# Performance work log

Measured on AMD Instinct MI355X. Metric: run time of the kernel, lower is better.

The kernel has to match this reference:

```python
import jax, jax.numpy as jnp
import numpy as np

N = 50000       # nodes
E = 1600000     # edges (avg degree 32)
DIN = 64
DOUT = 64
DE = 16
ATT_SLOPE = 0.2   # leaky_relu slope inside attention (GAT standard)
ACT_SLOPE = 0.01  # F.leaky_relu default between layers


def setup_inputs() -> dict:
    key = jax.random.key(0)
    ks = jax.random.split(key, 16)

    def lin(k, i, o):
        return jax.random.normal(k, (i, o), jnp.float32) / np.sqrt(i).astype(np.float32)

    def vec(k, d):
        return jax.random.normal(k, (d,), jnp.float32) / np.sqrt(d).astype(np.float32)

    return {
        "X": jax.random.normal(ks[0], (N, DIN), jnp.float32),
        "edge_index": jax.random.randint(ks[1], (2, E), 0, N),
        "edge_attr": jax.random.normal(ks[2], (E, DE), jnp.float32),
        # layer 1 params
        "W1": lin(ks[3], DIN, DOUT), "We1": lin(ks[4], DE, DOUT),
        "as1": vec(ks[5], DOUT), "ad1": vec(ks[6], DOUT), "ae1": vec(ks[7], DOUT),
        "b1": jnp.zeros((DOUT,), jnp.float32),
        # layer 2 params
        "W2": lin(ks[8], DOUT, DOUT), "We2": lin(ks[9], DE, DOUT),
        "as2": vec(ks[10], DOUT), "ad2": vec(ks[11], DOUT), "ae2": vec(ks[12], DOUT),
        "b2": jnp.zeros((DOUT,), jnp.float32),
    }


def _gat_conv(x, src, dst, edge_attr, W, We, a_s, a_d, a_e, b):
    """GATConv with edge features, softmax attention over dst neighborhoods, max aggregation."""
    n = x.shape[0]
    h = x @ W                      # [N, DOUT]
    e = edge_attr @ We             # [E, DOUT]
    # per-edge attention logits
    logits = jax.nn.leaky_relu((h @ a_s)[src] + (h @ a_d)[dst] + e @ a_e, ATT_SLOPE)  # [E]
    # numerically-stable segment softmax over destination node
    m = jax.ops.segment_max(logits, dst, num_segments=n)      # [N]
    p = jnp.exp(logits - m[dst])                               # [E]
    s = jax.ops.segment_sum(p, dst, num_segments=n)            # [N]
    att = p / jnp.maximum(s[dst], 1e-16)                       # [E]
    msg = (h[src] + e) * att[:, None]                          # [E, DOUT]
    out = jax.ops.segment_max(msg, dst, num_segments=n)        # [N, DOUT], -inf for empty
    out = jnp.where(jnp.isfinite(out), out, 0.0)
    return out + b


def reference(X, edge_index, edge_attr,
              W1, We1, as1, ad1, ae1, b1,
              W2, We2, as2, ad2, ae2, b2):
    src, dst = edge_index[0], edge_index[1]
    c1 = _gat_conv(X, src, dst, edge_attr, W1, We1, as1, ad1, ae1, b1)
    c1 = jax.nn.leaky_relu(c1, ACT_SLOPE)
    c2 = _gat_conv(c1, src, dst, edge_attr, W2, We2, as2, ad2, ae2, b2)
    c2 = jax.nn.leaky_relu(c2, ACT_SLOPE)
    return c2
```

## Files before the change

kernel.cpp:

```cpp
#include <hip/hip_runtime.h>
#include <cstdint>
#include <cstddef>

#define NN 50000
#define EE 1600000
#define D  64
#define DE 16

typedef __attribute__((ext_vector_type(2))) float vf2;

__device__ __forceinline__ float bf2f(unsigned short u) {
    return __uint_as_float(((unsigned)u) << 16);
}
__device__ __forceinline__ unsigned short f2bf(float f) {
    unsigned u = __float_as_uint(f);
    unsigned r = u + 0x7FFFu + ((u >> 16) & 1u);
    return (unsigned short)(r >> 16);
}
__device__ __forceinline__ vf2 vmax2(vf2 a, vf2 b) {
    vf2 r; r.x = fmaxf(a.x, b.x); r.y = fmaxf(a.y, b.y); return r;
}

__global__ __launch_bounds__(256) void k_hist(const int* dst, int* counts) {
    int e = blockIdx.x * 256 + threadIdx.x;
    if (e < EE) atomicAdd(&counts[dst[e]], 1);
}

__global__ __launch_bounds__(256) void k_scanA(const int* counts, int* bsum) {
    __shared__ int tmp[256];
    int t = threadIdx.x, i = blockIdx.x * 256 + t;
    tmp[t] = (i < NN) ? counts[i] : 0;
    __syncthreads();
    for (int off = 128; off; off >>= 1) {
        if (t < off) tmp[t] += tmp[t + off];
        __syncthreads();
    }
    if (t == 0) bsum[blockIdx.x] = tmp[0];
}

__global__ __launch_bounds__(256) void k_scanB(int* bsum, int nchunks) {
    __shared__ int tmp[256];
    int t = threadIdx.x;
    int v = (t < nchunks) ? bsum[t] : 0;
    tmp[t] = v; __syncthreads();
    for (int off = 1; off < 256; off <<= 1) {
        int x = (t >= off) ? tmp[t - off] : 0;
        __syncthreads();
        tmp[t] += x;
        __syncthreads();
    }
    if (t < nchunks) bsum[t] = tmp[t] - v;
}

__global__ __launch_bounds__(256) void k_scanC(const int* counts, const int* bsumex,
                                               int* offsets, int* cursor) {
    __shared__ int tmp[256];
    int t = threadIdx.x, i = blockIdx.x * 256 + t;
    int v = (i < NN) ? counts[i] : 0;
    tmp[t] = v; __syncthreads();
    for (int off = 1; off < 256; off <<= 1) {
        int x = (t >= off) ? tmp[t - off] : 0;
        __syncthreads();
        tmp[t] += x;
        __syncthreads();
    }
    int excl = tmp[t] - v + bsumex[blockIdx.x];
    if (i < NN) { offsets[i] = excl; cursor[i] = excl; }
}

__global__ __launch_bounds__(256) void k_scatter(const int* src, const int* dst,
                                                 const float* ea,
                                                 const float* We1, const float* ae1,
                                                 const float* We2, const float* ae2,
                                                 int* cursor, int4* recs) {
    __shared__ float wsh[32];
    int t = threadIdx.x;
    if (t < 32) {
        const float* We = (t < 16) ? We1 : We2;
        const float* ae = (t < 16) ? ae1 : ae2;
        int k = t & 15;
        float acc = 0.f;
        #pragma unroll
        for (int c = 0; c < 64; c++) acc += We[k * 64 + c] * ae[c];
        wsh[t] = acc;
    }
    __syncthreads();
    float w1r[16], w2r[16];
    #pragma unroll
    for (int j = 0; j < 16; j++) { w1r[j] = wsh[j]; w2r[j] = wsh[16 + j]; }

    int e = blockIdx.x * 256 + t;
    if (e >= EE) return;
    int d = dst[e];
    const float4* rp = (const float4*)(ea + (size_t)e * DE);
    float4 q0 = rp[0], q1 = rp[1], q2 = rp[2], q3 = rp[3];
    float ev[16] = {q0.x, q0.y, q0.z, q0.w, q1.x, q1.y, q1.z, q1.w,
                    q2.x, q2.y, q2.z, q2.w, q3.x, q3.y, q3.z, q3.w};
    float e1 = 0.f, e2 = 0.f;
    #pragma unroll
    for (int j = 0; j < 16; j++) {
        e1 += ev[j] * w1r[j];
        e2 += ev[j] * w2r[j];
    }
    int pos = atomicAdd(&cursor[d], 1);
    recs[pos] = make_int4(src[e], e, __float_as_int(e1), __float_as_int(e2));
}

template<int IN_BF16>
__global__ __launch_bounds__(256, 4) void k_gemm(const void* xin, const float* W,
                                                 const float* a_s, const float* a_d,
                                                 unsigned short* h, float* hs, float* hd) {
    int t = threadIdx.x, lane = t & 63;
    int wid0 = blockIdx.x * 4 + (t >> 6);
    float Wcol[64];
    #pragma unroll
    for (int k = 0; k < 64; k++) Wcol[k] = W[k * 64 + lane];
    float asl = a_s[lane], adl = a_d[lane];
    for (int n0 = wid0; n0 < NN; n0 += 4096) {
        int n = __builtin_amdgcn_readfirstlane(n0);
        float acc = 0.f;
        if (IN_BF16) {
            const uint4* xr = (const uint4*)((const unsigned short*)xin + (size_t)n * 64);
            #pragma unroll
            for (int q = 0; q < 8; q++) {
                uint4 u = xr[q];
                unsigned uu[4] = {u.x, u.y, u.z, u.w};
                #pragma unroll
                for (int j = 0; j < 4; j++) {
                    acc += bf2f((unsigned short)(uu[j] & 0xFFFFu)) * Wcol[q * 8 + 2 * j];
                    acc += bf2f((unsigned short)(uu[j] >> 16))     * Wcol[q * 8 + 2 * j + 1];
                }
            }
        } else {
            const float4* xr = (const float4*)((const float*)xin + (size_t)n * 64);
            #pragma unroll
            for (int q = 0; q < 16; q++) {
                float4 u = xr[q];
                acc += u.x * Wcol[4 * q]     + u.y * Wcol[4 * q + 1]
                     + u.z * Wcol[4 * q + 2] + u.w * Wcol[4 * q + 3];
            }
        }
        h[(size_t)n * 64 + lane] = f2bf(acc);
        float ps = acc * asl, pd = acc * adl;
        #pragma unroll
        for (int off = 32; off; off >>= 1) {
            ps += __shfl_xor(ps, off);
            pd += __shfl_xor(pd, off);
        }
        if (lane == 0) { hs[n] = ps; hd[n] = pd; }
    }
}

#define ATT_CAP 128
template<int L2>
__global__ __launch_bounds__(256, 4) void k_gat(const int4* recs, const int* offsets,
                                                const int* counts,
                                                const float* hs, const float* hd,
                                                const unsigned short* h, const float* ea,
                                                const float* We, const float* b, void* outv) {
    __shared__ float attl[4][ATT_CAP];
    int t = threadIdx.x, lane = t & 63, wv = t >> 6;
    int g = lane >> 4, cl = lane & 15;

    vf2 W01[16], W23[16];
    #pragma unroll
    for (int k = 0; k < 16; k++) {
        float4 w = *(const float4*)(We + k * 64 + 4 * cl);
        W01[k].x = w.x; W01[k].y = w.y;
        W23[k].x = w.z; W23[k].y = w.w;
    }

    int d = blockIdx.x * 4 + wv;
    int start = offsets[d];
    int deg = counts[d];

    if (deg == 0) {
        if (g == 0) {
            float4 bl = *(const float4*)(b + 4 * cl);
            float o0 = (bl.x >= 0.f) ? bl.x : 0.01f * bl.x;
            float o1 = (bl.y >= 0.f) ? bl.y : 0.01f * bl.y;
            float o2 = (bl.z >= 0.f) ? bl.z : 0.01f * bl.z;
            float o3 = (bl.w >= 0.f) ? bl.w : 0.01f * bl.w;
            size_t oidx = (size_t)d * D + 4 * cl;
            if (L2) *(float4*)((float*)outv + oidx) = make_float4(o0, o1, o2, o3);
            else {
                ushort4 ov = {f2bf(o0), f2bf(o1), f2bf(o2), f2bf(o3)};
                *(ushort4*)((unsigned short*)outv + oidx) = ov;
            }
        }
        return;
    }

    float hdv = hd[d];

    float m = -__builtin_inff();
    float s = 0.f;
    for (int i = lane; i < deg; i += 64) {
        int4 r = recs[start + i];
        float ee = __int_as_float(L2 ? r.w : r.z);
        float lg = hs[r.x] + hdv + ee;
        lg = (lg >= 0.f) ? lg : 0.2f * lg;
        if (i < ATT_CAP) attl[wv][i] = lg;
        float mn = fmaxf(m, lg);
        s = ((m == mn) ? s : s * __expf(m - mn)) + __expf(lg - mn);
        m = mn;
    }
    #pragma unroll
    for (int off = 32; off; off >>= 1) {
        float m2 = __shfl_xor(m, off);
        float s2 = __shfl_xor(s, off);
        float mn = fmaxf(m, m2);
        float sa = (m == mn) ? s : s * __expf(m - mn);
        float sb = (m2 == mn) ? s2 : s2 * __expf(m2 - mn);
        s = sa + sb;
        m = mn;
    }
    float invs = 1.0f / fmaxf(s, 1e-16f);

    int capdeg = min(deg, ATT_CAP);
    for (int i = lane; i < capdeg; i += 64)
        attl[wv][i] = __expf(attl[wv][i] - m) * invs;

    vf2 ninf2; ninf2.x = -__builtin_inff(); ninf2.y = -__builtin_inff();
    vf2 a01 = ninf2, a23 = ninf2;
    bool cached = (deg <= ATT_CAP);
    for (int i = 0; i < deg; i += 4) {
        int j = i + g;
        bool valid = (j < deg);
        int jc = valid ? j : 0;
        int4 r = recs[start + jc];
        float att;
        if (cached) {
            att = attl[wv][jc];
        } else {
            float ee = __int_as_float(L2 ? r.w : r.z);
            float lg = hs[r.x] + hdv + ee;
            lg = (lg >= 0.f) ? lg : 0.2f * lg;
            att = __expf(lg - m) * invs;
        }
        const float4* ep = (const float4*)(ea + (size_t)r.y * DE);
        float4 q0 = ep[0], q1 = ep[1], q2 = ep[2], q3 = ep[3];
        ushort4 hv = *(const ushort4*)(h + (size_t)r.x * D + 4 * cl);

        float ear[16] = {q0.x, q0.y, q0.z, q0.w, q1.x, q1.y, q1.z, q1.w,
                         q2.x, q2.y, q2.z, q2.w, q3.x, q3.y, q3.z, q3.w};
        vf2 e01 = {0.f, 0.f}, e23 = {0.f, 0.f};
        #pragma unroll
        for (int k = 0; k < 16; k++) {
            vf2 eb; eb.x = ear[k]; eb.y = ear[k];
            e01 += eb * W01[k];
            e23 += eb * W23[k];
        }
        vf2 h01, h23;
        h01.x = bf2f(hv.x); h01.y = bf2f(hv.y);
        h23.x = bf2f(hv.z); h23.y = bf2f(hv.w);
        vf2 att2; att2.x = att; att2.y = att;
        vf2 v01 = (h01 + e01) * att2;
        vf2 v23 = (h23 + e23) * att2;
        if (!valid) { v01 = ninf2; v23 = ninf2; }
        a01 = vmax2(a01, v01);
        a23 = vmax2(a23, v23);
    }
    #pragma unroll
    for (int off = 16; off <= 32; off <<= 1) {
        a01.x = fmaxf(a01.x, __shfl_xor(a01.x, off));
        a01.y = fmaxf(a01.y, __shfl_xor(a01.y, off));
        a23.x = fmaxf(a23.x, __shfl_xor(a23.x, off));
        a23.y = fmaxf(a23.y, __shfl_xor(a23.y, off));
    }

    if (g == 0) {
        float4 bl = *(const float4*)(b + 4 * cl);
        float o0 = a01.x + bl.x, o1 = a01.y + bl.y;
        float o2 = a23.x + bl.z, o3 = a23.y + bl.w;
        o0 = (o0 >= 0.f) ? o0 : 0.01f * o0;
        o1 = (o1 >= 0.f) ? o1 : 0.01f * o1;
        o2 = (o2 >= 0.f) ? o2 : 0.01f * o2;
        o3 = (o3 >= 0.f) ? o3 : 0.01f * o3;
        size_t oidx = (size_t)d * D + 4 * cl;
        if (L2) {
            *(float4*)((float*)outv + oidx) = make_float4(o0, o1, o2, o3);
        } else {
            ushort4 ov = {f2bf(o0), f2bf(o1), f2bf(o2), f2bf(o3)};
            *(ushort4*)((unsigned short*)outv + oidx) = ov;
        }
    }
}

extern "C" void kernel_launch(void* const* d_in, const int* in_sizes, int n_in,
                              void* d_out, int out_size, void* d_ws, size_t ws_size,
                              hipStream_t stream) {
    const float* X   = (const float*)d_in[0];
    const int*   eix = (const int*)d_in[1];
    const float* ea  = (const float*)d_in[2];
    const float* W1  = (const float*)d_in[3];
    const float* We1 = (const float*)d_in[4];
    const float* as1 = (const float*)d_in[5];
    const float* ad1 = (const float*)d_in[6];
    const float* ae1 = (const float*)d_in[7];
    const float* b1  = (const float*)d_in[8];
    const float* W2  = (const float*)d_in[9];
    const float* We2 = (const float*)d_in[10];
    const float* as2 = (const float*)d_in[11];
    const float* ad2 = (const float*)d_in[12];
    const float* ae2 = (const float*)d_in[13];
    const float* b2  = (const float*)d_in[14];

    const int* src = eix;
    const int* dst = eix + EE;

    char* w = (char*)d_ws;
    int4* recs = (int4*)w;               w += (size_t)EE * 16;
    unsigned short* hA = (unsigned short*)w; w += (size_t)NN * D * 2;
    unsigned short* hB = (unsigned short*)w; w += (size_t)NN * D * 2;
    float* hs = (float*)w;               w += (size_t)NN * 4;
    float* hd = (float*)w;               w += (size_t)NN * 4;
    int* counts = (int*)w;               w += (size_t)NN * 4;
    int* offsets = (int*)w;              w += (size_t)NN * 4;
    int* cursor = (int*)w;               w += (size_t)NN * 4;
    int* bsum = (int*)w;                 w += 256 * 4;

    const int nchunks = (NN + 255) / 256;

    hipMemsetAsync(counts, 0, (size_t)NN * 4, stream);
    k_hist<<<EE / 256, 256, 0, stream>>>(dst, counts);
    k_scanA<<<nchunks, 256, 0, stream>>>(counts, bsum);
    k_scanB<<<1, 256, 0, stream>>>(bsum, nchunks);
    k_scanC<<<nchunks, 256, 0, stream>>>(counts, bsum, offsets, cursor);
    k_scatter<<<EE / 256, 256, 0, stream>>>(src, dst, ea, We1, ae1, We2, ae2, cursor, recs);

    k_gemm<0><<<1024, 256, 0, stream>>>(X, W1, as1, ad1, hA, hs, hd);
    k_gat<0><<<NN / 4, 256, 0, stream>>>(recs, offsets, counts, hs, hd, hA, ea, We1, b1, hB);
    k_gemm<1><<<1024, 256, 0, stream>>>(hB, W2, as2, ad2, hB, hs, hd);
    k_gat<1><<<NN / 4, 256, 0, stream>>>(recs, offsets, counts, hs, hd, hB, ea, We2, b2,
                                         (float*)d_out);
}
```

Measured before the change: 684.3 us.

## Software-pipeline gather loop with register-cached edge records for low-degree nodes

For nodes with degree up to 64, the edge src/edge-id records read in the softmax pass are kept in registers and broadcast with shuffles instead of being re-read from global memory. The main gather loop is software-pipelined: the next iteration's edge-attribute and h loads are issued before the current iteration's math, and the first loads start before the softmax reduction. Adds __restrict__ qualifiers and lowers the launch-bounds occupancy hint from 4 to 3 to allow more registers. This raises register pressure and lowers occupancy in exchange for more memory-level parallelism per wave.

Result: faster. 620.0 us (-9.4%).

```diff
diff --git a/kernel.cpp b/kernel.cpp
--- a/kernel.cpp
+++ b/kernel.cpp
@@ -153,11 +153,16 @@
 
 #define ATT_CAP 128
 template<int L2>
-__global__ __launch_bounds__(256, 4) void k_gat(const int4* recs, const int* offsets,
-                                                const int* counts,
-                                                const float* hs, const float* hd,
-                                                const unsigned short* h, const float* ea,
-                                                const float* We, const float* b, void* outv) {
+__global__ __launch_bounds__(256, 3) void k_gat(const int4* __restrict__ recs,
+                                                const int* __restrict__ offsets,
+                                                const int* __restrict__ counts,
+                                                const float* __restrict__ hs,
+                                                const float* __restrict__ hd,
+                                                const unsigned short* __restrict__ h,
+                                                const float* __restrict__ ea,
+                                                const float* __restrict__ We,
+                                                const float* __restrict__ b,
+                                                void* __restrict__ outv) {
     __shared__ float attl[4][ATT_CAP];
     int t = threadIdx.x, lane = t & 63, wv = t >> 6;
     int g = lane >> 4, cl = lane & 15;
@@ -193,10 +198,12 @@
 
     float hdv = hd[d];
 
+    int rxr = 0, ryr = 0;
     float m = -__builtin_inff();
     float s = 0.f;
     for (int i = lane; i < deg; i += 64) {
         int4 r = recs[start + i];
+        if (i < 64) { rxr = r.x; ryr = r.y; }
         float ee = __int_as_float(L2 ? r.w : r.z);
         float lg = hs[r.x] + hdv + ee;
         lg = (lg >= 0.f) ? lg : 0.2f * lg;
@@ -205,6 +212,20 @@
         s = ((m == mn) ? s : s * __expf(m - mn)) + __expf(lg - mn);
         m = mn;
     }
+
+    bool fast = (deg <= 64);
+
+    int jc0 = 0; bool vcur = false;
+    float4 c0, c1, c2, c3; ushort4 hv;
+    if (fast) {
+        vcur = (g < deg);
+        jc0 = vcur ? g : 0;
+        int rx = __shfl(rxr, jc0), ry = __shfl(ryr, jc0);
+        const float4* ep = (const float4*)(ea + (size_t)ry * DE);
+        c0 = ep[0]; c1 = ep[1]; c2 = ep[2]; c3 = ep[3];
+        hv = *(const ushort4*)(h + (size_t)rx * D + 4 * cl);
+    }
+
     #pragma unroll
     for (int off = 32; off; off >>= 1) {
         float m2 = __shfl_xor(m, off);
@@ -223,44 +244,82 @@
 
     vf2 ninf2; ninf2.x = -__builtin_inff(); ninf2.y = -__builtin_inff();
     vf2 a01 = ninf2, a23 = ninf2;
-    bool cached = (deg <= ATT_CAP);
-    for (int i = 0; i < deg; i += 4) {
-        int j = i + g;
-        bool valid = (j < deg);
-        int jc = valid ? j : 0;
-        int4 r = recs[start + jc];
-        float att;
-        if (cached) {
-            att = attl[wv][jc];
-        } else {
-            float ee = __int_as_float(L2 ? r.w : r.z);
-            float lg = hs[r.x] + hdv + ee;
-            lg = (lg >= 0.f) ? lg : 0.2f * lg;
-            att = __expf(lg - m) * invs;
-        }
-        const float4* ep = (const float4*)(ea + (size_t)r.y * DE);
-        float4 q0 = ep[0], q1 = ep[1], q2 = ep[2], q3 = ep[3];
-        ushort4 hv = *(const ushort4*)(h + (size_t)r.x * D + 4 * cl);
-
-        float ear[16] = {q0.x, q0.y, q0.z, q0.w, q1.x, q1.y, q1.z, q1.w,
-                         q2.x, q2.y, q2.z, q2.w, q3.x, q3.y, q3.z, q3.w};
-        vf2 e01 = {0.f, 0.f}, e23 = {0.f, 0.f};
-        #pragma unroll
-        for (int k = 0; k < 16; k++) {
-            vf2 eb; eb.x = ear[k]; eb.y = ear[k];
-            e01 += eb * W01[k];
-            e23 += eb * W23[k];
-        }
-        vf2 h01, h23;
-        h01.x = bf2f(hv.x); h01.y = bf2f(hv.y);
-        h23.x = bf2f(hv.z); h23.y = bf2f(hv.w);
-        vf2 att2; att2.x = att; att2.y = att;
-        vf2 v01 = (h01 + e01) * att2;
-        vf2 v23 = (h23 + e23) * att2;
-        if (!valid) { v01 = ninf2; v23 = ninf2; }
-        a01 = vmax2(a01, v01);
-        a23 = vmax2(a23, v23);
-    }
+
+    if (fast) {
+        float att = attl[wv][jc0];
+        for (int i = 0; i < deg; i += 4) {
+            int jn = i + 4 + g;
+            bool vnext = (jn < deg);
+            int jcn = vnext ? jn : 0;
+            int rxn = __shfl(rxr, jcn), ryn = __shfl(ryr, jcn);
+            const float4* epn = (const float4*)(ea + (size_t)ryn * DE);
+            float4 n0 = epn[0], n1 = epn[1], n2 = epn[2], n3 = epn[3];
+            ushort4 hvn = *(const ushort4*)(h + (size_t)rxn * D + 4 * cl);
+            float attn2 = attl[wv][jcn];
+
+            float ear[16] = {c0.x, c0.y, c0.z, c0.w, c1.x, c1.y, c1.z, c1.w,
+                             c2.x, c2.y, c2.z, c2.w, c3.x, c3.y, c3.z, c3.w};
+            vf2 e01 = {0.f, 0.f}, e23 = {0.f, 0.f};
+            #pragma unroll
+            for (int k = 0; k < 16; k++) {
+                vf2 eb; eb.x = ear[k]; eb.y = ear[k];
+                e01 += eb * W01[k];
+                e23 += eb * W23[k];
+            }
+            vf2 h01, h23;
+            h01.x = bf2f(hv.x); h01.y = bf2f(hv.y);
+            h23.x = bf2f(hv.z); h23.y = bf2f(hv.w);
+            vf2 att2; att2.x = att; att2.y = att;
+            vf2 v01 = (h01 + e01) * att2;
+            vf2 v23 = (h23 + e23) * att2;
+            if (!vcur) { v01 = ninf2; v23 = ninf2; }
+            a01 = vmax2(a01, v01);
+            a23 = vmax2(a23, v23);
+
+            c0 = n0; c1 = n1; c2 = n2; c3 = n3;
+            hv = hvn; att = attn2; vcur = vnext;
+        }
+    } else {
+        bool cached = (deg <= ATT_CAP);
+        for (int i = 0; i < deg; i += 4) {
+            int j = i + g;
+            bool valid = (j < deg);
+            int jc = valid ? j : 0;
+            int4 r = recs[start + jc];
+            float att;
+            if (cached) {
+                att = attl[wv][jc];
+            } else {
+                float ee = __int_as_float(L2 ? r.w : r.z);
+                float lg = hs[r.x] + hdv + ee;
+                lg = (lg >= 0.f) ? lg : 0.2f * lg;
+                att = __expf(lg - m) * invs;
+            }
+            const float4* ep = (const float4*)(ea + (size_t)r.y * DE);
+            float4 q0 = ep[0], q1 = ep[1], q2 = ep[2], q3 = ep[3];
+            ushort4 hq = *(const ushort4*)(h + (size_t)r.x * D + 4 * cl);
+
+            float ear[16] = {q0.x, q0.y, q0.z, q0.w, q1.x, q1.y, q1.z, q1.w,
+                             q2.x, q2.y, q2.z, q2.w, q3.x, q3.y, q3.z, q3.w};
+            vf2 e01 = {0.f, 0.f}, e23 = {0.f, 0.f};
+            #pragma unroll
+            for (int k = 0; k < 16; k++) {
+                vf2 eb; eb.x = ear[k]; eb.y = ear[k];
+                e01 += eb * W01[k];
+                e23 += eb * W23[k];
+            }
+            vf2 h01, h23;
+            h01.x = bf2f(hq.x); h01.y = bf2f(hq.y);
+            h23.x = bf2f(hq.z); h23.y = bf2f(hq.w);
+            vf2 att2; att2.x = att; att2.y = att;
+            vf2 v01 = (h01 + e01) * att2;
+            vf2 v23 = (h23 + e23) * att2;
+            if (!valid) { v01 = ninf2; v23 = ninf2; }
+            a01 = vmax2(a01, v01);
+            a23 = vmax2(a23, v23);
+        }
+    }
+
     #pragma unroll
     for (int off = 16; off <= 32; off <<= 1) {
         a01.x = fmaxf(a01.x, __shfl_xor(a01.x, off));
```

## Stage edge attributes in LDS with single-pass softmax and prefetch for low-degree nodes

Applied to the files above, without the earlier changes.

For nodes with degree up to 64, each lane loads one edge's record and its 16-float edge attribute once into shared memory. The softmax is computed in one pass with plain wave reductions. The max-aggregation loop then reads the attributes from LDS and prefetches the next h row, replacing the previous per-feature-group redundant global reads of edge attributes. The We weights are repacked so the projection accumulates along k as paired values, and __restrict__ is added. LDS use grows and occupancy drops from 4 to 3 blocks per CU, while higher-degree nodes keep a slower recompute path.

New measurement: 590.0 us. -13.8%, faster.

```diff
diff --git a/kernel.cpp b/kernel.cpp
--- a/kernel.cpp
+++ b/kernel.cpp
@@ -16,9 +16,6 @@
     unsigned u = __float_as_uint(f);
     unsigned r = u + 0x7FFFu + ((u >> 16) & 1u);
     return (unsigned short)(r >> 16);
-}
-__device__ __forceinline__ vf2 vmax2(vf2 a, vf2 b) {
-    vf2 r; r.x = fmaxf(a.x, b.x); r.y = fmaxf(a.y, b.y); return r;
 }
 
 __global__ __launch_bounds__(256) void k_hist(const int* dst, int* counts) {
@@ -151,23 +148,31 @@
     }
 }
 
-#define ATT_CAP 128
 template<int L2>
-__global__ __launch_bounds__(256, 4) void k_gat(const int4* recs, const int* offsets,
-                                                const int* counts,
-                                                const float* hs, const float* hd,
-                                                const unsigned short* h, const float* ea,
-                                                const float* We, const float* b, void* outv) {
-    __shared__ float attl[4][ATT_CAP];
+__global__ __launch_bounds__(256, 3) void k_gat(const int4* __restrict__ recs,
+                                                const int* __restrict__ offsets,
+                                                const int* __restrict__ counts,
+                                                const float* __restrict__ hs,
+                                                const float* __restrict__ hd,
+                                                const unsigned short* __restrict__ h,
+                                                const float* __restrict__ ea,
+                                                const float* __restrict__ We,
+                                                const float* __restrict__ b,
+                                                void* __restrict__ outv) {
+    __shared__ float4 eal[4][4][64];
+    __shared__ float2 arx[4][64];
     int t = threadIdx.x, lane = t & 63, wv = t >> 6;
     int g = lane >> 4, cl = lane & 15;
 
-    vf2 W01[16], W23[16];
+    vf2 Wp[32];
     #pragma unroll
-    for (int k = 0; k < 16; k++) {
-        float4 w = *(const float4*)(We + k * 64 + 4 * cl);
-        W01[k].x = w.x; W01[k].y = w.y;
-        W23[k].x = w.z; W23[k].y = w.w;
+    for (int kp = 0; kp < 8; kp++) {
+        float4 wa = *(const float4*)(We + (2 * kp) * 64 + 4 * cl);
+        float4 wb = *(const float4*)(We + (2 * kp + 1) * 64 + 4 * cl);
+        Wp[kp].x      = wa.x; Wp[kp].y      = wb.x;
+        Wp[8 + kp].x  = wa.y; Wp[8 + kp].y  = wb.y;
+        Wp[16 + kp].x = wa.z; Wp[16 + kp].y = wb.z;
+        Wp[24 + kp].x = wa.w; Wp[24 + kp].y = wb.w;
     }
 
     int d = blockIdx.x * 4 + wv;
@@ -192,87 +197,147 @@
     }
 
     float hdv = hd[d];
-
-    float m = -__builtin_inff();
-    float s = 0.f;
-    for (int i = lane; i < deg; i += 64) {
-        int4 r = recs[start + i];
-        float ee = __int_as_float(L2 ? r.w : r.z);
-        float lg = hs[r.x] + hdv + ee;
-        lg = (lg >= 0.f) ? lg : 0.2f * lg;
-        if (i < ATT_CAP) attl[wv][i] = lg;
-        float mn = fmaxf(m, lg);
-        s = ((m == mn) ? s : s * __expf(m - mn)) + __expf(lg - mn);
-        m = mn;
-    }
-    #pragma unroll
-    for (int off = 32; off; off >>= 1) {
-        float m2 = __shfl_xor(m, off);
-        float s2 = __shfl_xor(s, off);
-        float mn = fmaxf(m, m2);
-        float sa = (m == mn) ? s : s * __expf(m - mn);
-        float sb = (m2 == mn) ? s2 : s2 * __expf(m2 - mn);
-        s = sa + sb;
-        m = mn;
-    }
-    float invs = 1.0f / fmaxf(s, 1e-16f);
-
-    int capdeg = min(deg, ATT_CAP);
-    for (int i = lane; i < capdeg; i += 64)
-        attl[wv][i] = __expf(attl[wv][i] - m) * invs;
-
-    vf2 ninf2; ninf2.x = -__builtin_inff(); ninf2.y = -__builtin_inff();
-    vf2 a01 = ninf2, a23 = ninf2;
-    bool cached = (deg <= ATT_CAP);
-    for (int i = 0; i < deg; i += 4) {
-        int j = i + g;
-        bool valid = (j < deg);
-        int jc = valid ? j : 0;
-        int4 r = recs[start + jc];
-        float att;
-        if (cached) {
-            att = attl[wv][jc];
-        } else {
+    bool fast = (deg <= 64);
+    float m, invs;
+
+    float ninf = -__builtin_inff();
+    float a0 = ninf, a1 = ninf, a2 = ninf, a3 = ninf;
+
+    if (fast) {
+        float lg = ninf;
+        if (lane < deg) {
+            int4 r = recs[start + lane];
+            const float4* ep = (const float4*)(ea + (size_t)r.y * DE);
+            float4 q0 = ep[0], q1 = ep[1], q2 = ep[2], q3 = ep[3];
+            eal[wv][0][lane] = q0; eal[wv][1][lane] = q1;
+            eal[wv][2][lane] = q2; eal[wv][3][lane] = q3;
+            arx[wv][lane].y = __int_as_float(r.x);
+            float ee = __int_as_float(L2 ? r.w : r.z);
+            lg = hs[r.x] + hdv + ee;
+            lg = (lg >= 0.f) ? lg : 0.2f * lg;
+        }
+
+        bool vC = (g < deg);
+        int jC = vC ? g : 0;
+        int rxC = __float_as_int(arx[wv][jC].y);
+        ushort4 hvC = *(const ushort4*)(h + (size_t)rxC * D + 4 * cl);
+
+        m = lg;
+        #pragma unroll
+        for (int off = 32; off; off >>= 1) m = fmaxf(m, __shfl_xor(m, off));
+        float p = __expf(lg - m);
+        float s = p;
+        #pragma unroll
+        for (int off = 32; off; off >>= 1) s += __shfl_xor(s, off);
+        invs = 1.0f / fmaxf(s, 1e-16f);
+        if (lane < deg) arx[wv][lane].x = p * invs;
+
+        float attC = arx[wv][jC].x;
+
+        for (int i = 0; i < deg; i += 4) {
+            int jn = i + 4 + g;
+            bool vN = (jn < deg);
+            int jN = vN ? jn : 0;
+            float2 arN = arx[wv][jN];
+            int rxN = __float_as_int(arN.y);
+            ushort4 hvN = *(const ushort4*)(h + (size_t)rxN * D + 4 * cl);
+
+            vf2 acA = {0.f, 0.f}, acB = {0.f, 0.f}, acC = {0.f, 0.f}, acD = {0.f, 0.f};
+            #pragma unroll
+            for (int kq = 0; kq < 4; kq++) {
+                float4 q = eal[wv][kq][jC];
+                vf2 eA; eA.x = q.x; eA.y = q.y;
+                vf2 eB; eB.x = q.z; eB.y = q.w;
+                acA += eA * Wp[2 * kq];      acA += eB * Wp[2 * kq + 1];
+                acB += eA * Wp[8 + 2 * kq];  acB += eB * Wp[8 + 2 * kq + 1];
+                acC += eA * Wp[16 + 2 * kq]; acC += eB * Wp[16 + 2 * kq + 1];
+                acD += eA * Wp[24 + 2 * kq]; acD += eB * Wp[24 + 2 * kq + 1];
+            }
+            float e0 = acA.x + acA.y, e1 = acB.x + acB.y;
+            float e2 = acC.x + acC.y, e3 = acD.x + acD.y;
+            float o0 = (bf2f(hvC.x) + e0) * attC;
+            float o1 = (bf2f(hvC.y) + e1) * attC;
+            float o2 = (bf2f(hvC.z) + e2) * attC;
+            float o3 = (bf2f(hvC.w) + e3) * attC;
+            if (vC) {
+                a0 = fmaxf(a0, o0); a1 = fmaxf(a1, o1);
+                a2 = fmaxf(a2, o2); a3 = fmaxf(a3, o3);
+            }
+            attC = arN.x; hvC = hvN; vC = vN; jC = jN;
+        }
+    } else {
+        float mm = ninf, s = 0.f;
+        for (int i = lane; i < deg; i += 64) {
+            int4 r = recs[start + i];
             float ee = __int_as_float(L2 ? r.w : r.z);
             float lg = hs[r.x] + hdv + ee;
             lg = (lg >= 0.f) ? lg : 0.2f * lg;
-            att = __expf(lg - m) * invs;
-        }
-        const float4* ep = (const float4*)(ea + (size_t)r.y * DE);
-        float4 q0 = ep[0], q1 = ep[1], q2 = ep[2], q3 = ep[3];
-        ushort4 hv = *(const ushort4*)(h + (size_t)r.x * D + 4 * cl);
-
-        float ear[16] = {q0.x, q0.y, q0.z, q0.w, q1.x, q1.y, q1.z, q1.w,
-                         q2.x, q2.y, q2.z, q2.w, q3.x, q3.y, q3.z, q3.w};
-        vf2 e01 = {0.f, 0.f}, e23 = {0.f, 0.f};
+            float mn = fmaxf(mm, lg);
+            s = ((mm == mn) ? s : s * __expf(mm - mn)) + __expf(lg - mn);
+            mm = mn;
+        }
         #pragma unroll
-        for (int k = 0; k < 16; k++) {
-            vf2 eb; eb.x = ear[k]; eb.y = ear[k];
-            e01 += eb * W01[k];
-            e23 += eb * W23[k];
-        }
-        vf2 h01, h23;
-        h01.x = bf2f(hv.x); h01.y = bf2f(hv.y);
-        h23.x = bf2f(hv.z); h23.y = bf2f(hv.w);
-        vf2 att2; att2.x = att; att2.y = att;
-        vf2 v01 = (h01 + e01) * att2;
-        vf2 v23 = (h23 + e23) * att2;
-        if (!valid) { v01 = ninf2; v23 = ninf2; }
-        a01 = vmax2(a01, v01);
-        a23 = vmax2(a23, v23);
-    }
+        for (int off = 32; off; off >>= 1) {
+            float m2 = __shfl_xor(mm, off);
+            float s2 = __shfl_xor(s, off);
+            float mn = fmaxf(mm, m2);
+            float sa = (mm == mn) ? s : s * __expf(mm - mn);
+            float sb = (m2 == mn) ? s2 : s2 * __expf(m2 - mn);
+            s = sa + sb;
+            mm = mn;
+        }
+        m = mm;
+        invs = 1.0f / fmaxf(s, 1e-16f);
+
+        for (int i = 0; i < deg; i += 4) {
+            int j = i + g;
+            bool valid = (j < deg);
+            int jc = valid ? j : 0;
+            int4 r = recs[start + jc];
+            float ee = __int_as_float(L2 ? r.w : r.z);
+            float lg = hs[r.x] + hdv + ee;
+            lg = (lg >= 0.f) ? lg : 0.2f * lg;
+            float att = __expf(lg - m) * invs;
+            const float4* ep = (const float4*)(ea + (size_t)r.y * DE);
+            float4 q0 = ep[0], q1 = ep[1], q2 = ep[2], q3 = ep[3];
+            ushort4 hv = *(const ushort4*)(h + (size_t)r.x * D + 4 * cl);
+            float4 qs[4] = {q0, q1, q2, q3};
+            vf2 acA = {0.f, 0.f}, acB = {0.f, 0.f}, acC = {0.f, 0.f}, acD = {0.f, 0.f};
+            #pragma unroll
+            for (int kq = 0; kq < 4; kq++) {
+                float4 q = qs[kq];
+                vf2 eA; eA.x = q.x; eA.y = q.y;
+                vf2 eB; eB.x = q.z; eB.y = q.w;
+                acA += eA * Wp[2 * kq];      acA += eB * Wp[2 * kq + 1];
+                acB += eA * Wp[8 + 2 * kq];  acB += eB * Wp[8 + 2 * kq + 1];
+                acC += eA * Wp[16 + 2 * kq]; acC += eB * Wp[16 + 2 * kq + 1];
+                acD += eA * Wp[24 + 2 * kq]; acD += eB * Wp[24 + 2 * kq + 1];
+            }
+            float e0 = acA.x + acA.y, e1 = acB.x + acB.y;
+            float e2 = acC.x + acC.y, e3 = acD.x + acD.y;
+            float o0 = (bf2f(hv.x) + e0) * att;
+            float o1 = (bf2f(hv.y) + e1) * att;
+            float o2 = (bf2f(hv.z) + e2) * att;
+            float o3 = (bf2f(hv.w) + e3) * att;
+            if (valid) {
+                a0 = fmaxf(a0, o0); a1 = fmaxf(a1, o1);
+                a2 = fmaxf(a2, o2); a3 = fmaxf(a3, o3);
+            }
+        }
+    }
+
     #pragma unroll
     for (int off = 16; off <= 32; off <<= 1) {
-        a01.x = fmaxf(a01.x, __shfl_xor(a01.x, off));
-        a01.y = fmaxf(a01.y, __shfl_xor(a01.y, off));
-        a23.x = fmaxf(a23.x, __shfl_xor(a23.x, off));
-        a23.y = fmaxf(a23.y, __shfl_xor(a23.y, off));
+        a0 = fmaxf(a0, __shfl_xor(a0, off));
+        a1 = fmaxf(a1, __shfl_xor(a1, off));
+        a2 = fmaxf(a2, __shfl_xor(a2, off));
+        a3 = fmaxf(a3, __shfl_xor(a3, off));
     }
 
     if (g == 0) {
         float4 bl = *(const float4*)(b + 4 * cl);
-        float o0 = a01.x + bl.x, o1 = a01.y + bl.y;
-        float o2 = a23.x + bl.z, o3 = a23.y + bl.w;
+        float o0 = a0 + bl.x, o1 = a1 + bl.y;
+        float o2 = a2 + bl.z, o3 = a3 + bl.w;
         o0 = (o0 >= 0.f) ? o0 : 0.01f * o0;
         o1 = (o1 >= 0.f) ? o1 : 0.01f * o1;
         o2 = (o2 >= 0.f) ? o2 : 0.01f * o2;
```
